# Kernel optimization log

Hardware: AMD Instinct MI355X
Metric: run time of the kernel (lower is better)

## Reference

```python
import jax, jax.numpy as jnp
import numpy as np

FILTER_WIDTH = 23
NSIG = 9.0
RATIO = 4.0
SUB_LOW_RATIO = 1.0
PCT = 3.0  # normalization_percentile_threshold


def _gaussian_kernel_2d(ksize, sigma):
    # matches cv2.getGaussianKernel for sigma > 0: normalized 1D gaussian, outer product
    i = np.arange(ksize, dtype=np.float64) - (ksize - 1) / 2.0
    k1 = np.exp(-(i ** 2) / (2.0 * sigma ** 2))
    k1 /= k1.sum()
    k2 = np.outer(k1, k1)
    return k2.astype(np.float32)


def setup_inputs() -> dict:
    key = jax.random.key(0)
    k1, k2 = jax.random.split(key)
    x = jax.random.normal(k1, (16, 3, 512, 512), dtype=jnp.float32)
    mask = jax.random.uniform(k2, (16, 1, 512, 512), dtype=jnp.float32)
    kernel = jnp.asarray(_gaussian_kernel_2d(FILTER_WIDTH, NSIG))[None, None]  # [1,1,23,23]
    return {"x": x, "mask": mask, "kernel": kernel}


def reference(x, mask, kernel):
    N, C, H, W = x.shape
    pad = FILTER_WIDTH // 2  # 11

    # --- median padding (torch.median = lower median -> sorted index (n-1)//2) ---
    flat = x.reshape(N, C, H * W)
    med = jnp.sort(flat, axis=-1)[:, :, (H * W - 1) // 2] + 0.2  # [N,C]
    med = med[:, :, None, None]
    xp = mask * x + (1.0 - mask) * med  # [N,C,H,W]

    # --- Gaussian low-pass: replication pad + depthwise conv (same kernel per channel) ---
    xpad = jnp.pad(xp, ((0, 0), (0, 0), (pad, pad), (pad, pad)), mode="edge")
    k = jnp.broadcast_to(kernel, (C, 1, FILTER_WIDTH, FILTER_WIDTH))
    gauss = jax.lax.conv_general_dilated(
        xpad, k, window_strides=(1, 1), padding="VALID", feature_group_count=C
    )  # [N,C,H,W]

    res = RATIO * (xp - SUB_LOW_RATIO * gauss)

    # --- per-(n,c) percentile normalization on 1/256-quantized copy ---
    temp = jnp.trunc(res * 256.0) / 256.0  # torch .int() truncates toward zero
    tflat = temp.reshape(N, C, H * W)
    lo = jnp.percentile(tflat, PCT, axis=-1)[:, :, None, None]
    hi = jnp.percentile(tflat, 100.0 - PCT, axis=-1)[:, :, None, None]
    res = (res - lo) / (hi - lo)

    # sub_mask=True
    return res * mask
```

## Files before the change

### kernel.cpp

```cpp
#include <hip/hip_runtime.h>

#define HW 262144
#define WID 512
#define PLANES 48
#define NCH 3
#define PAD 11
#define FW 23
#define XS 92
#define NSUB 16

__device__ __forceinline__ float uniform_f(float v) {
  return __uint_as_float((unsigned)__builtin_amdgcn_readfirstlane((int)__float_as_uint(v)));
}

__global__ __launch_bounds__(512, 4) void hist1_kernel(const float* __restrict__ x,
                                                       ushort* __restrict__ part) {
  __shared__ int h[8192];
  const int p = blockIdx.x, s = blockIdx.y, tid = threadIdx.x;
  for (int i = tid; i < 8192; i += 512) h[i] = 0;
  __syncthreads();
  const float4* xv = (const float4*)(x + (size_t)p * HW + (size_t)s * (HW / NSUB));
  float4 a[8];
#pragma unroll
  for (int q = 0; q < 8; ++q) a[q] = xv[tid + q * 512];
#define H1(c) { int bin = (int)(((c) + 8.0f) * 512.0f); bin = min(max(bin, 0), 8191); atomicAdd(&h[bin], 1); }
#pragma unroll
  for (int q = 0; q < 8; ++q) { H1(a[q].x); H1(a[q].y); H1(a[q].z); H1(a[q].w); }
#undef H1
  __syncthreads();
  uint4* out = (uint4*)(part + ((size_t)p * NSUB + s) * 8192);
  for (int k = tid; k < 1024; k += 512) {
    int4 c = *(const int4*)&h[k * 8];
    int4 d = *(const int4*)&h[k * 8 + 4];
    uint4 w;
    w.x = (unsigned)c.x | ((unsigned)c.y << 16);
    w.y = (unsigned)c.z | ((unsigned)c.w << 16);
    w.z = (unsigned)d.x | ((unsigned)d.y << 16);
    w.w = (unsigned)d.z | ((unsigned)d.w << 16);
    out[k] = w;
  }
}

__global__ __launch_bounds__(256) void scan_med_kernel(const ushort* __restrict__ part,
                                                       float* __restrict__ med,
                                                       const float* __restrict__ kern,
                                                       float* __restrict__ k1g) {
  __shared__ int hsum[8192];
  __shared__ int incl[256];
  __shared__ int s_chunk, s_base;
  const int p = blockIdx.x, t = threadIdx.x;
  if (p == 0 && t < FW) k1g[t] = kern[t * FW + PAD] / sqrtf(kern[PAD * FW + PAD]);
  const uint4* pr = (const uint4*)(part + (size_t)p * NSUB * 8192);
  for (int idx = t; idx < 1024; idx += 256) {
    int a0=0,a1=0,a2=0,a3=0,a4=0,a5=0,a6=0,a7=0;
#pragma unroll
    for (int s = 0; s < NSUB; ++s) {
      uint4 v = pr[(size_t)s * 1024 + idx];
      a0 += (int)(v.x & 0xffff); a1 += (int)(v.x >> 16);
      a2 += (int)(v.y & 0xffff); a3 += (int)(v.y >> 16);
      a4 += (int)(v.z & 0xffff); a5 += (int)(v.z >> 16);
      a6 += (int)(v.w & 0xffff); a7 += (int)(v.w >> 16);
    }
    int* hb = &hsum[idx * 8];
    hb[0]=a0; hb[1]=a1; hb[2]=a2; hb[3]=a3; hb[4]=a4; hb[5]=a5; hb[6]=a6; hb[7]=a7;
  }
  __syncthreads();
  int mysum = 0;
#pragma unroll
  for (int j = 0; j < 32; j += 4) {
    int4 v = *(const int4*)&hsum[t * 32 + j];
    mysum += v.x + v.y + v.z + v.w;
  }
  incl[t] = mysum;
  __syncthreads();
  for (int off = 1; off < 256; off <<= 1) {
    int v = (t >= off) ? incl[t - off] : 0;
    __syncthreads();
    incl[t] += v;
    __syncthreads();
  }
  const int rank = 131072;
  {
    int excl = incl[t] - mysum;
    if (excl < rank && rank <= incl[t]) { s_chunk = t; s_base = rank - excl; }
  }
  __syncthreads();
  if (t < 64) {
    const int c = s_chunk, base = s_base;
    int cnt = (t < 32) ? hsum[c * 32 + t] : 0;
    int pfx = cnt;
#pragma unroll
    for (int off = 1; off < 32; off <<= 1) {
      int u = __shfl_up(pfx, off, 64);
      if (t >= off) pfx += u;
    }
    unsigned long long m = __ballot(t < 32 && pfx >= base);
    int bin = c * 32 + (__ffsll((long long)m) - 1);
    if (t == 0) med[p] = -8.0f + ((float)bin + 0.5f) * 0.001953125f + 0.2f;
  }
}

__global__ __launch_bounds__(256) void conv_kernel(const float* __restrict__ x,
                                                   const float* __restrict__ mask,
                                                   const float* __restrict__ k1g,
                                                   const float* __restrict__ med,
                                                   float* __restrict__ res) {
  __shared__ float xs[86 * XS];
  const int tid = threadIdx.x;

  const int tt = (blockIdx.x & 7) * 384 + (blockIdx.x >> 3);
  const int z = tt >> 6;
  const int tby = (tt >> 3) & 7, tbx = tt & 7;
  const int n = z / NCH;

  float k1[FW];
#pragma unroll
  for (int t = 0; t < FW; ++t) k1[t] = uniform_f(k1g[t]);

  const float m_med = uniform_f(med[z]);
  const int gr0 = tby * 64 - PAD;
  const int gc0 = tbx * 64 - PAD;
  const float* xb = x + (size_t)z * HW;
  const float* mb = mask + (size_t)n * HW;
  for (int i = tid; i < 86 * 86; i += 256) {
    int r = i / 86, c = i - r * 86;
    int gr = min(max(gr0 + r, 0), WID - 1);
    int gc = min(max(gc0 + c, 0), WID - 1);
    int g = gr * WID + gc;
    float xv = xb[g], mv = mb[g];
    xs[r * XS + c] = fmaf(mv, xv - m_med, m_med);
  }
  __syncthreads();

  float ah[3][8];
#pragma unroll
  for (int it = 0; it < 3; ++it) {
    const int g = tid + (it << 8);
    if (g < 86 * 8) {
      const int r = g >> 3, c0 = (g & 7) << 3;
      const float* row = &xs[r * XS + c0];
      float w[32];
#pragma unroll
      for (int q = 0; q < 8; ++q) *(float4*)&w[q * 4] = *(const float4*)(row + q * 4);
#pragma unroll
      for (int j = 0; j < 8; ++j) ah[it][j] = 0.f;
#pragma unroll
      for (int t = 0; t < FW; ++t) {
        const float k = k1[t];
#pragma unroll
        for (int j = 0; j < 8; ++j) ah[it][j] = fmaf(k, w[t + j], ah[it][j]);
      }
    }
  }

  const int ct = (tid & 15) << 2;
  const int rt = (tid >> 4) << 2;
  float4 xpA[4], xpB[4];
#pragma unroll
  for (int j = 0; j < 4; ++j) {
    const float* xr = &xs[(rt + j + PAD) * XS + ct];
    xpA[j] = *(const float4*)(xr + 8);
    xpB[j] = *(const float4*)(xr + 12);
  }
  __syncthreads();

#pragma unroll
  for (int it = 0; it < 3; ++it) {
    const int g = tid + (it << 8);
    if (g < 86 * 8) {
      const int r = g >> 3, c0 = (g & 7) << 3;
      *(float4*)&xs[r * XS + c0] = make_float4(ah[it][0], ah[it][1], ah[it][2], ah[it][3]);
      *(float4*)&xs[r * XS + c0 + 4] = make_float4(ah[it][4], ah[it][5], ah[it][6], ah[it][7]);
    }
  }
  __syncthreads();

  float4 acc[4];
#pragma unroll
  for (int j = 0; j < 4; ++j) acc[j] = make_float4(0.f, 0.f, 0.f, 0.f);
#pragma unroll
  for (int tp = 0; tp < 26; ++tp) {
    float4 v = *(const float4*)&xs[(rt + tp) * XS + ct];
    const int jlo = (tp - 22 > 0) ? (tp - 22) : 0;
    const int jhi = (tp < 3) ? tp : 3;
#pragma unroll
    for (int j = jlo; j <= jhi; ++j) {
      float k = k1[tp - j];
      acc[j].x = fmaf(k, v.x, acc[j].x);
      acc[j].y = fmaf(k, v.y, acc[j].y);
      acc[j].z = fmaf(k, v.z, acc[j].z);
      acc[j].w = fmaf(k, v.w, acc[j].w);
    }
  }

  float* rb = res + (size_t)z * HW + (size_t)(tby * 64 + rt) * WID + tbx * 64 + ct;
#pragma unroll
  for (int j = 0; j < 4; ++j) {
    float4 o;
    o.x = 4.0f * (xpA[j].w - acc[j].x);
    o.y = 4.0f * (xpB[j].x - acc[j].y);
    o.z = 4.0f * (xpB[j].y - acc[j].z);
    o.w = 4.0f * (xpB[j].z - acc[j].w);
    *(float4*)(rb + (size_t)j * WID) = o;
  }
}

__global__ __launch_bounds__(512, 4) void hist_kernel(const float* __restrict__ res,
                                                      ushort* __restrict__ part) {
  __shared__ int h[8192];
  const int b = blockIdx.x;
  const int xcd = b & 7, idx = b >> 3;
  const int p = xcd * 6 + (idx >> 4);
  const int s = idx & 15;
  const int tid = threadIdx.x;
  for (int i = tid; i < 8192; i += 512) h[i] = 0;
  __syncthreads();
  const float4* rv = (const float4*)(res + (size_t)p * HW + (size_t)s * (HW / NSUB));
  float4 a[8];
#pragma unroll
  for (int q = 0; q < 8; ++q) a[q] = rv[tid + q * 512];
#define HADD(c) { int bin = (int)((c) * 256.0f) + 4096; bin = min(max(bin, 0), 8191); atomicAdd(&h[bin], 1); }
#pragma unroll
  for (int q = 0; q < 8; ++q) { HADD(a[q].x); HADD(a[q].y); HADD(a[q].z); HADD(a[q].w); }
#undef HADD
  __syncthreads();
  uint4* out = (uint4*)(part + ((size_t)p * NSUB + s) * 8192);
  for (int k = tid; k < 1024; k += 512) {
    int4 c = *(const int4*)&h[k * 8];
    int4 d = *(const int4*)&h[k * 8 + 4];
    uint4 w;
    w.x = (unsigned)c.x | ((unsigned)c.y << 16);
    w.y = (unsigned)c.z | ((unsigned)c.w << 16);
    w.z = (unsigned)d.x | ((unsigned)d.y << 16);
    w.w = (unsigned)d.z | ((unsigned)d.w << 16);
    out[k] = w;
  }
}

__global__ __launch_bounds__(256) void pct_kernel(const ushort* __restrict__ part,
                                                  float* __restrict__ lo_out,
                                                  float* __restrict__ inv_out) {
  __shared__ int hsum[8192];
  __shared__ int incl[256];
  __shared__ int s_chunk, s_base;
  __shared__ float s_v[4];
  const int p = blockIdx.x, t = threadIdx.x;
  const uint4* pr = (const uint4*)(part + (size_t)p * NSUB * 8192);
  for (int idx = t; idx < 1024; idx += 256) {
    int a0=0,a1=0,a2=0,a3=0,a4=0,a5=0,a6=0,a7=0;
#pragma unroll
    for (int s = 0; s < NSUB; ++s) {
      uint4 v = pr[(size_t)s * 1024 + idx];
      a0 += (int)(v.x & 0xffff); a1 += (int)(v.x >> 16);
      a2 += (int)(v.y & 0xffff); a3 += (int)(v.y >> 16);
      a4 += (int)(v.z & 0xffff); a5 += (int)(v.z >> 16);
      a6 += (int)(v.w & 0xffff); a7 += (int)(v.w >> 16);
    }
    int* hb = &hsum[idx * 8];
    hb[0]=a0; hb[1]=a1; hb[2]=a2; hb[3]=a3; hb[4]=a4; hb[5]=a5; hb[6]=a6; hb[7]=a7;
  }
  __syncthreads();
  int mysum = 0;
#pragma unroll
  for (int j = 0; j < 32; j += 4) {
    int4 v = *(const int4*)&hsum[t * 32 + j];
    mysum += v.x + v.y + v.z + v.w;
  }
  incl[t] = mysum;
  __syncthreads();
  for (int off = 1; off < 256; off <<= 1) {
    int v = (t >= off) ? incl[t - off] : 0;
    __syncthreads();
    incl[t] += v;
    __syncthreads();
  }
  const int ranks[4] = {7865, 7866, 254279, 254280};
#pragma unroll
  for (int r = 0; r < 4; ++r) {
    const int rank = ranks[r];
    int excl = incl[t] - mysum;
    if (excl < rank && rank <= incl[t]) { s_chunk = t; s_base = rank - excl; }
    __syncthreads();
    if (t < 64) {
      const int c = s_chunk, base = s_base;
      int cnt = (t < 32) ? hsum[c * 32 + t] : 0;
      int pfx = cnt;
#pragma unroll
      for (int off = 1; off < 32; off <<= 1) {
        int u = __shfl_up(pfx, off, 64);
        if (t >= off) pfx += u;
      }
      unsigned long long m = __ballot(t < 32 && pfx >= base);
      int bin = c * 32 + (__ffsll((long long)m) - 1);
      if (t == 0) s_v[r] = (float)(bin - 4096) * 0.00390625f;
    }
    __syncthreads();
  }
  if (t == 0) {
    const double fl = 0.29, fh = 0.71;
    double lov = (double)s_v[0] + fl * ((double)s_v[1] - (double)s_v[0]);
    double hiv = (double)s_v[2] + fh * ((double)s_v[3] - (double)s_v[2]);
    lo_out[p] = (float)lov;
    inv_out[p] = (float)(1.0 / (hiv - lov));
  }
}

__global__ __launch_bounds__(256) void final_kernel(float* __restrict__ res,
                                                    const float* __restrict__ mask,
                                                    const float* __restrict__ lo,
                                                    const float* __restrict__ inv) {
  const int b = blockIdx.x;
  const int xcd = b & 7, idx = b >> 3;
  const int z = xcd * 6 + (idx >> 6);
  const int chunk = idx & 63;
  const int n = z / NCH;
  const int base = z * 65536 + chunk * 1024 + threadIdx.x;
  const int h0 = base & 65535;
  float4* rz = (float4*)res;
  const float4* mz = (const float4*)mask + (size_t)n * 65536;
  float4 r0 = rz[base],       r1 = rz[base + 256],
         r2 = rz[base + 512], r3 = rz[base + 768];
  float4 m0 = mz[h0],       m1 = mz[h0 + 256],
         m2 = mz[h0 + 512], m3 = mz[h0 + 768];
  const float l = lo[z];
  const float iv = inv[z];
  float4 o0, o1, o2, o3;
  o0.x = (r0.x - l) * iv * m0.x;  o0.y = (r0.y - l) * iv * m0.y;
  o0.z = (r0.z - l) * iv * m0.z;  o0.w = (r0.w - l) * iv * m0.w;
  o1.x = (r1.x - l) * iv * m1.x;  o1.y = (r1.y - l) * iv * m1.y;
  o1.z = (r1.z - l) * iv * m1.z;  o1.w = (r1.w - l) * iv * m1.w;
  o2.x = (r2.x - l) * iv * m2.x;  o2.y = (r2.y - l) * iv * m2.y;
  o2.z = (r2.z - l) * iv * m2.z;  o2.w = (r2.w - l) * iv * m2.w;
  o3.x = (r3.x - l) * iv * m3.x;  o3.y = (r3.y - l) * iv * m3.y;
  o3.z = (r3.z - l) * iv * m3.z;  o3.w = (r3.w - l) * iv * m3.w;
  rz[base] = o0;
  rz[base + 256] = o1;
  rz[base + 512] = o2;
  rz[base + 768] = o3;
}

extern "C" void kernel_launch(void* const* d_in, const int* in_sizes, int n_in,
                              void* d_out, int out_size, void* d_ws, size_t ws_size,
                              hipStream_t stream) {
  (void)in_sizes; (void)n_in; (void)out_size; (void)ws_size;
  const float* x = (const float*)d_in[0];
  const float* mask = (const float*)d_in[1];
  const float* kern = (const float*)d_in[2];
  float* out = (float*)d_out;

  ushort* part = (ushort*)d_ws;
  float* med = (float*)(part + (size_t)PLANES * NSUB * 8192);
  float* lo = med + PLANES;
  float* inv = lo + PLANES;
  float* k1g = inv + PLANES;

  hist1_kernel<<<dim3(PLANES, NSUB), 512, 0, stream>>>(x, part);
  scan_med_kernel<<<PLANES, 256, 0, stream>>>(part, med, kern, k1g);
  conv_kernel<<<dim3(3072), 256, 0, stream>>>(x, mask, k1g, med, out);
  hist_kernel<<<dim3(768), 512, 0, stream>>>(out, part);
  pct_kernel<<<PLANES, 256, 0, stream>>>(part, lo, inv);
  final_kernel<<<dim3(3072), 256, 0, stream>>>(out, mask, lo, inv);
}
```

Before: 187.9 us.

## Fuse partial histogram and scan kernels into single per-plane block kernels

Replaces the two-stage histogram (many sub-blocks writing packed partial histograms, then a per-plane reduce/scan kernel) with one 1024-thread block per plane that builds the full LDS histogram and selects the median or percentiles directly. This removes two kernel launches and the workspace round-trip of partial histograms. In exchange only 48 blocks run, so most CUs sit idle and each block streams a full 1 MB plane with heavier LDS atomic contention.

```diff
diff --git a/kernel.cpp b/kernel.cpp
--- a/kernel.cpp
+++ b/kernel.cpp
@@ -7,96 +7,73 @@
 #define PAD 11
 #define FW 23
 #define XS 92
-#define NSUB 16
 
 __device__ __forceinline__ float uniform_f(float v) {
   return __uint_as_float((unsigned)__builtin_amdgcn_readfirstlane((int)__float_as_uint(v)));
 }
 
-__global__ __launch_bounds__(512, 4) void hist1_kernel(const float* __restrict__ x,
-                                                       ushort* __restrict__ part) {
+__global__ __launch_bounds__(1024) void med_kernel(const float* __restrict__ x,
+                                                   float* __restrict__ med,
+                                                   const float* __restrict__ kern,
+                                                   float* __restrict__ k1g) {
   __shared__ int h[8192];
-  const int p = blockIdx.x, s = blockIdx.y, tid = threadIdx.x;
-  for (int i = tid; i < 8192; i += 512) h[i] = 0;
-  __syncthreads();
-  const float4* xv = (const float4*)(x + (size_t)p * HW + (size_t)s * (HW / NSUB));
-  float4 a[8];
-#pragma unroll
-  for (int q = 0; q < 8; ++q) a[q] = xv[tid + q * 512];
-#define H1(c) { int bin = (int)(((c) + 8.0f) * 512.0f); bin = min(max(bin, 0), 8191); atomicAdd(&h[bin], 1); }
-#pragma unroll
-  for (int q = 0; q < 8; ++q) { H1(a[q].x); H1(a[q].y); H1(a[q].z); H1(a[q].w); }
-#undef H1
-  __syncthreads();
-  uint4* out = (uint4*)(part + ((size_t)p * NSUB + s) * 8192);
-  for (int k = tid; k < 1024; k += 512) {
-    int4 c = *(const int4*)&h[k * 8];
-    int4 d = *(const int4*)&h[k * 8 + 4];
-    uint4 w;
-    w.x = (unsigned)c.x | ((unsigned)c.y << 16);
-    w.y = (unsigned)c.z | ((unsigned)c.w << 16);
-    w.z = (unsigned)d.x | ((unsigned)d.y << 16);
-    w.w = (unsigned)d.z | ((unsigned)d.w << 16);
-    out[k] = w;
-  }
-}
-
-__global__ __launch_bounds__(256) void scan_med_kernel(const ushort* __restrict__ part,
-                                                       float* __restrict__ med,
-                                                       const float* __restrict__ kern,
-                                                       float* __restrict__ k1g) {
-  __shared__ int hsum[8192];
   __shared__ int incl[256];
   __shared__ int s_chunk, s_base;
-  const int p = blockIdx.x, t = threadIdx.x;
-  if (p == 0 && t < FW) k1g[t] = kern[t * FW + PAD] / sqrtf(kern[PAD * FW + PAD]);
-  const uint4* pr = (const uint4*)(part + (size_t)p * NSUB * 8192);
-  for (int idx = t; idx < 1024; idx += 256) {
-    int a0=0,a1=0,a2=0,a3=0,a4=0,a5=0,a6=0,a7=0;
-#pragma unroll
-    for (int s = 0; s < NSUB; ++s) {
-      uint4 v = pr[(size_t)s * 1024 + idx];
-      a0 += (int)(v.x & 0xffff); a1 += (int)(v.x >> 16);
-      a2 += (int)(v.y & 0xffff); a3 += (int)(v.y >> 16);
-      a4 += (int)(v.z & 0xffff); a5 += (int)(v.z >> 16);
-      a6 += (int)(v.w & 0xffff); a7 += (int)(v.w >> 16);
-    }
-    int* hb = &hsum[idx * 8];
-    hb[0]=a0; hb[1]=a1; hb[2]=a2; hb[3]=a3; hb[4]=a4; hb[5]=a5; hb[6]=a6; hb[7]=a7;
-  }
+  const int b = blockIdx.x;
+  const int p = (b & 7) * 6 + (b >> 3);
+  const int tid = threadIdx.x;
+  if (p == 0 && tid < FW) k1g[tid] = kern[tid * FW + PAD] / sqrtf(kern[PAD * FW + PAD]);
+  for (int i = tid; i < 8192; i += 1024) h[i] = 0;
+  __syncthreads();
+  const float4* xv = (const float4*)(x + (size_t)p * HW);
+#define H1(c) { int bin = (int)(((c) + 8.0f) * 512.0f); bin = min(max(bin, 0), 8191); atomicAdd(&h[bin], 1); }
+  for (int rb = 0; rb < 8; rb += 2) {
+    float4 a[8], c[8];
+#pragma unroll
+    for (int q = 0; q < 8; ++q) a[q] = xv[tid + (rb * 8 + q) * 1024];
+#pragma unroll
+    for (int q = 0; q < 8; ++q) c[q] = xv[tid + (rb * 8 + 8 + q) * 1024];
+#pragma unroll
+    for (int q = 0; q < 8; ++q) { H1(a[q].x); H1(a[q].y); H1(a[q].z); H1(a[q].w); }
+#pragma unroll
+    for (int q = 0; q < 8; ++q) { H1(c[q].x); H1(c[q].y); H1(c[q].z); H1(c[q].w); }
+  }
+#undef H1
   __syncthreads();
   int mysum = 0;
-#pragma unroll
-  for (int j = 0; j < 32; j += 4) {
-    int4 v = *(const int4*)&hsum[t * 32 + j];
-    mysum += v.x + v.y + v.z + v.w;
-  }
-  incl[t] = mysum;
+  if (tid < 256) {
+#pragma unroll
+    for (int j = 0; j < 32; j += 4) {
+      int4 v = *(const int4*)&h[tid * 32 + j];
+      mysum += v.x + v.y + v.z + v.w;
+    }
+    incl[tid] = mysum;
+  }
   __syncthreads();
   for (int off = 1; off < 256; off <<= 1) {
-    int v = (t >= off) ? incl[t - off] : 0;
-    __syncthreads();
-    incl[t] += v;
+    int v = (tid < 256 && tid >= off) ? incl[tid - off] : 0;
+    __syncthreads();
+    if (tid < 256) incl[tid] += v;
     __syncthreads();
   }
   const int rank = 131072;
-  {
-    int excl = incl[t] - mysum;
-    if (excl < rank && rank <= incl[t]) { s_chunk = t; s_base = rank - excl; }
-  }
-  __syncthreads();
-  if (t < 64) {
+  if (tid < 256) {
+    int excl = incl[tid] - mysum;
+    if (excl < rank && rank <= incl[tid]) { s_chunk = tid; s_base = rank - excl; }
+  }
+  __syncthreads();
+  if (tid < 64) {
     const int c = s_chunk, base = s_base;
-    int cnt = (t < 32) ? hsum[c * 32 + t] : 0;
+    int cnt = (tid < 32) ? h[c * 32 + tid] : 0;
     int pfx = cnt;
 #pragma unroll
     for (int off = 1; off < 32; off <<= 1) {
       int u = __shfl_up(pfx, off, 64);
-      if (t >= off) pfx += u;
-    }
-    unsigned long long m = __ballot(t < 32 && pfx >= base);
+      if (tid >= off) pfx += u;
+    }
+    unsigned long long m = __ballot(tid < 32 && pfx >= base);
     int bin = c * 32 + (__ffsll((long long)m) - 1);
-    if (t == 0) med[p] = -8.0f + ((float)bin + 0.5f) * 0.001953125f + 0.2f;
+    if (tid == 0) med[p] = -8.0f + ((float)bin + 0.5f) * 0.001953125f + 0.2f;
   }
 }
 
@@ -205,98 +182,74 @@
   }
 }
 
-__global__ __launch_bounds__(512, 4) void hist_kernel(const float* __restrict__ res,
-                                                      ushort* __restrict__ part) {
+__global__ __launch_bounds__(1024) void pct_kernel(const float* __restrict__ res,
+                                                   float* __restrict__ lo_out,
+                                                   float* __restrict__ inv_out) {
   __shared__ int h[8192];
-  const int b = blockIdx.x;
-  const int xcd = b & 7, idx = b >> 3;
-  const int p = xcd * 6 + (idx >> 4);
-  const int s = idx & 15;
-  const int tid = threadIdx.x;
-  for (int i = tid; i < 8192; i += 512) h[i] = 0;
-  __syncthreads();
-  const float4* rv = (const float4*)(res + (size_t)p * HW + (size_t)s * (HW / NSUB));
-  float4 a[8];
-#pragma unroll
-  for (int q = 0; q < 8; ++q) a[q] = rv[tid + q * 512];
-#define HADD(c) { int bin = (int)((c) * 256.0f) + 4096; bin = min(max(bin, 0), 8191); atomicAdd(&h[bin], 1); }
-#pragma unroll
-  for (int q = 0; q < 8; ++q) { HADD(a[q].x); HADD(a[q].y); HADD(a[q].z); HADD(a[q].w); }
-#undef HADD
-  __syncthreads();
-  uint4* out = (uint4*)(part + ((size_t)p * NSUB + s) * 8192);
-  for (int k = tid; k < 1024; k += 512) {
-    int4 c = *(const int4*)&h[k * 8];
-    int4 d = *(const int4*)&h[k * 8 + 4];
-    uint4 w;
-    w.x = (unsigned)c.x | ((unsigned)c.y << 16);
-    w.y = (unsigned)c.z | ((unsigned)c.w << 16);
-    w.z = (unsigned)d.x | ((unsigned)d.y << 16);
-    w.w = (unsigned)d.z | ((unsigned)d.w << 16);
-    out[k] = w;
-  }
-}
-
-__global__ __launch_bounds__(256) void pct_kernel(const ushort* __restrict__ part,
-                                                  float* __restrict__ lo_out,
-                                                  float* __restrict__ inv_out) {
-  __shared__ int hsum[8192];
   __shared__ int incl[256];
   __shared__ int s_chunk, s_base;
   __shared__ float s_v[4];
-  const int p = blockIdx.x, t = threadIdx.x;
-  const uint4* pr = (const uint4*)(part + (size_t)p * NSUB * 8192);
-  for (int idx = t; idx < 1024; idx += 256) {
-    int a0=0,a1=0,a2=0,a3=0,a4=0,a5=0,a6=0,a7=0;
-#pragma unroll
-    for (int s = 0; s < NSUB; ++s) {
-      uint4 v = pr[(size_t)s * 1024 + idx];
-      a0 += (int)(v.x & 0xffff); a1 += (int)(v.x >> 16);
-      a2 += (int)(v.y & 0xffff); a3 += (int)(v.y >> 16);
-      a4 += (int)(v.z & 0xffff); a5 += (int)(v.z >> 16);
-      a6 += (int)(v.w & 0xffff); a7 += (int)(v.w >> 16);
-    }
-    int* hb = &hsum[idx * 8];
-    hb[0]=a0; hb[1]=a1; hb[2]=a2; hb[3]=a3; hb[4]=a4; hb[5]=a5; hb[6]=a6; hb[7]=a7;
-  }
+  const int b = blockIdx.x;
+  const int p = (b & 7) * 6 + (b >> 3);
+  const int tid = threadIdx.x;
+  for (int i = tid; i < 8192; i += 1024) h[i] = 0;
+  __syncthreads();
+  const float4* rv = (const float4*)(res + (size_t)p * HW);
+#define HADD(c) { int bin = (int)((c) * 256.0f) + 4096; bin = min(max(bin, 0), 8191); atomicAdd(&h[bin], 1); }
+  for (int rb = 0; rb < 8; rb += 2) {
+    float4 a[8], c[8];
+#pragma unroll
+    for (int q = 0; q < 8; ++q) a[q] = rv[tid + (rb * 8 + q) * 1024];
+#pragma unroll
+    for (int q = 0; q < 8; ++q) c[q] = rv[tid + (rb * 8 + 8 + q) * 1024];
+#pragma unroll
+    for (int q = 0; q < 8; ++q) { HADD(a[q].x); HADD(a[q].y); HADD(a[q].z); HADD(a[q].w); }
+#pragma unroll
+    for (int q = 0; q < 8; ++q) { HADD(c[q].x); HADD(c[q].y); HADD(c[q].z); HADD(c[q].w); }
+  }
+#undef HADD
   __syncthreads();
   int mysum = 0;
-#pragma unroll
-  for (int j = 0; j < 32; j += 4) {
-    int4 v = *(const int4*)&hsum[t * 32 + j];
-    mysum += v.x + v.y + v.z + v.w;
-  }
-  incl[t] = mysum;
+  if (tid < 256) {
+#pragma unroll
+    for (int j = 0; j < 32; j += 4) {
+      int4 v = *(const int4*)&h[tid * 32 + j];
+      mysum += v.x + v.y + v.z + v.w;
+    }
+    incl[tid] = mysum;
+  }
   __syncthreads();
   for (int off = 1; off < 256; off <<= 1) {
-    int v = (t >= off) ? incl[t - off] : 0;
-    __syncthreads();
-    incl[t] += v;
+    int v = (tid < 256 && tid >= off) ? incl[tid - off] : 0;
+    __syncthreads();
+    if (tid < 256) incl[tid] += v;
     __syncthreads();
   }
   const int ranks[4] = {7865, 7866, 254279, 254280};
 #pragma unroll
   for (int r = 0; r < 4; ++r) {
     const int rank = ranks[r];
-    int excl = incl[t] - mysum;
-    if (excl < rank && rank <= incl[t]) { s_chunk = t; s_base = rank - excl; }
-    __syncthreads();
-    if (t < 64) {
+    if (tid < 256) {
+      int excl = incl[tid] - mysum;
+      if (excl < rank && rank <= incl[tid]) { s_chunk = tid; s_base = rank - excl; }
+    }
+    __syncthreads();
+    if (tid < 64) {
       const int c = s_chunk, base = s_base;
-      int cnt = (t < 32) ? hsum[c * 32 + t] : 0;
+      int cnt = (tid < 32) ? h[c * 32 + tid] : 0;
       int pfx = cnt;
 #pragma unroll
       for (int off = 1; off < 32; off <<= 1) {
         int u = __shfl_up(pfx, off, 64);
-        if (t >= off) pfx += u;
+        if (tid >= off) pfx += u;
       }
-      unsigned long long m = __ballot(t < 32 && pfx >= base);
+      unsigned long long m = __ballot(tid < 32 && pfx >= base);
       int bin = c * 32 + (__ffsll((long long)m) - 1);
-      if (t == 0) s_v[r] = (float)(bin - 4096) * 0.00390625f;
-    }
-    __syncthreads();
-  }
-  if (t == 0) {
+      if (tid == 0) s_v[r] = (float)(bin - 4096) * 0.00390625f;
+    }
+    __syncthreads();
+  }
+  if (tid == 0) {
     const double fl = 0.29, fh = 0.71;
     double lov = (double)s_v[0] + fl * ((double)s_v[1] - (double)s_v[0]);
     double hiv = (double)s_v[2] + fh * ((double)s_v[3] - (double)s_v[2]);
@@ -348,16 +301,13 @@
   const float* kern = (const float*)d_in[2];
   float* out = (float*)d_out;
 
-  ushort* part = (ushort*)d_ws;
-  float* med = (float*)(part + (size_t)PLANES * NSUB * 8192);
+  float* med = (float*)d_ws;
   float* lo = med + PLANES;
   float* inv = lo + PLANES;
   float* k1g = inv + PLANES;
 
-  hist1_kernel<<<dim3(PLANES, NSUB), 512, 0, stream>>>(x, part);
-  scan_med_kernel<<<PLANES, 256, 0, stream>>>(part, med, kern, k1g);
+  med_kernel<<<dim3(PLANES), 1024, 0, stream>>>(x, med, kern, k1g);
   conv_kernel<<<dim3(3072), 256, 0, stream>>>(x, mask, k1g, med, out);
-  hist_kernel<<<dim3(768), 512, 0, stream>>>(out, part);
-  pct_kernel<<<PLANES, 256, 0, stream>>>(part, lo, inv);
+  pct_kernel<<<dim3(PLANES), 1024, 0, stream>>>(out, lo, inv);
   final_kernel<<<dim3(3072), 256, 0, stream>>>(out, mask, lo, inv);
 }
```

New measurement: 194.0 us. 3.3% more time.
